# Kernel tuning notes

Measured on AMD Instinct MI355X. Metric: run time of the kernel, lower is better.

## Reference

```python
import jax, jax.numpy as jnp
import numpy as np
import math

N_HEADS = 16
D_HEAD = 64
D_MODEL = 1024
ROPE_THETA = 10000.0


def setup_inputs() -> dict:
    key = jax.random.key(0)
    k1, k2, k3 = jax.random.split(key, 3)
    B, T = 2, 2048
    x = jax.random.normal(k1, (B, T, D_MODEL), dtype=jnp.float32)
    # torch Linear(in, out) weight has shape (out, in); store transposed (in, out)
    # so forward is x @ w. Scale like default init to keep activations sane.
    w_qkv = jax.random.normal(k2, (D_MODEL, 3 * D_MODEL), dtype=jnp.float32) / math.sqrt(D_MODEL)
    w_o = jax.random.normal(k3, (D_MODEL, D_MODEL), dtype=jnp.float32) / math.sqrt(D_MODEL)
    return {"x": x, "w_qkv": w_qkv, "w_o": w_o}


def _build_rope(T, dtype):
    inv_freq = 1.0 / (ROPE_THETA ** (jnp.arange(0, D_HEAD, 2, dtype=jnp.float32) / D_HEAD))
    t = jnp.arange(T, dtype=jnp.float32)
    freqs = jnp.outer(t, inv_freq)            # [T, D_HEAD/2]
    emb = jnp.concatenate([freqs, freqs], -1)  # [T, D_HEAD]
    return jnp.cos(emb).astype(dtype), jnp.sin(emb).astype(dtype)


def _apply_rope(x, cos, sin):
    # x: [B, T, H, D_HEAD]; cos/sin broadcast as [1, T, 1, D_HEAD]
    x1, x2 = jnp.split(x, 2, axis=-1)
    rotated = jnp.concatenate([-x2, x1], axis=-1)
    return x * cos + rotated * sin


def reference(x, w_qkv, w_o):
    B, T, D = x.shape
    qkv = (x @ w_qkv).reshape(B, T, 3, N_HEADS, D_HEAD)
    q, k, v = qkv[:, :, 0], qkv[:, :, 1], qkv[:, :, 2]  # [B, T, H, Dh]
    cos, sin = _build_rope(T, x.dtype)
    cos = cos[None, :, None, :]
    sin = sin[None, :, None, :]
    q = _apply_rope(q, cos, sin)
    k = _apply_rope(k, cos, sin)
    scale = 1.0 / math.sqrt(D_HEAD)
    # full [B, H, T, T] scores (faithful to the manual matmul-softmax-matmul)
    attn = jnp.einsum("bthd,bshd->bhts", q, k) * scale
    attn = jax.nn.softmax(attn, axis=-1)
    out = jnp.einsum("bhts,bshd->bthd", attn, v).reshape(B, T, D)
    return out @ w_o
```

## Files before the change

### kernel.cpp

```cpp
#include <hip/hip_runtime.h>
#include <cstdint>

typedef unsigned short ushort_t;
typedef __attribute__((ext_vector_type(8))) short v8s;
typedef __attribute__((ext_vector_type(4))) short v4s;
typedef __attribute__((ext_vector_type(2))) unsigned v2u;
typedef __attribute__((ext_vector_type(4))) float v4f;

#define MFMA(a, b, c) __builtin_amdgcn_mfma_f32_16x16x32_bf16(a, b, c, 0, 0, 0)
#define QSCALE 0.18033688011112042f

__device__ __forceinline__ float bf2f(ushort_t u) {
    union { unsigned u; float f; } x; x.u = ((unsigned)u) << 16; return x.f;
}
__device__ __forceinline__ short f2bf(float f) {
    union { float f; unsigned u; } x; x.f = f;
    unsigned r = x.u + 0x7fffu + ((x.u >> 16) & 1u);
    return (short)(r >> 16);
}

__global__ void detect_dtype(const unsigned* __restrict__ x, int* __restrict__ flag) {
    __shared__ int cnt;
    if (threadIdx.x == 0) cnt = 0;
    __syncthreads();
    unsigned w = x[threadIdx.x];
    int e = (w >> 7) & 0xFF;
    int hit = ((e >= 96 && e <= 135) || (w & 0xFFFFu) == 0) ? 1 : 0;
    atomicAdd(&cnt, hit);
    __syncthreads();
    if (threadIdx.x == 0) *flag = (cnt >= 160) ? 1 : 0;
}

__global__ __launch_bounds__(256) void cvt_x(const void* __restrict__ xin,
                                             ushort_t* __restrict__ xb,
                                             const int* __restrict__ flagp, int n8) {
    int i = blockIdx.x * 256 + threadIdx.x;
    if (i >= n8) return;
    if (*flagp) {
        ((v8s*)xb)[i] = ((const v8s*)xin)[i];
    } else {
        const float* xf = (const float*)xin + (size_t)i * 8;
        v8s o;
        #pragma unroll
        for (int j = 0; j < 8; ++j) o[j] = f2bf(xf[j]);
        ((v8s*)xb)[i] = o;
    }
}

__global__ __launch_bounds__(256) void cvt_transpose(const void* __restrict__ in,
                                                     ushort_t* __restrict__ out,
                                                     const int* __restrict__ flagp,
                                                     int R, int C) {
    __shared__ ushort_t tile[32][33];
    int bx = blockIdx.x * 32, by = blockIdx.y * 32;
    int tx = threadIdx.x, ty = threadIdx.y;
    int isbf = *flagp;
    for (int i = ty; i < 32; i += 8) {
        size_t idx = (size_t)(by + i) * C + bx + tx;
        tile[i][tx] = isbf ? ((const ushort_t*)in)[idx]
                           : (ushort_t)f2bf(((const float*)in)[idx]);
    }
    __syncthreads();
    for (int i = ty; i < 32; i += 8) out[(size_t)(bx + i) * R + by + tx] = tile[tx][i];
}

__global__ __launch_bounds__(256) void rope_table(float* __restrict__ tab) {
    int idx = blockIdx.x * 256 + threadIdx.x;
    int t = idx >> 5, d = idx & 31;
    float inv_freq = __expf(-(float)d * 0.28782313662425575f);
    float ang = (float)t * inv_freq;
    float sn, cs;
    sincosf(ang, &sn, &cs);
    tab[t * 64 + d]      = bf2f((ushort_t)f2bf(cs));
    tab[t * 64 + 32 + d] = bf2f((ushort_t)f2bf(sn));
}

template <int MODE>
__global__ __launch_bounds__(256) void gemm_bt(const ushort_t* __restrict__ A,
                                               const ushort_t* __restrict__ BT,
                                               void* __restrict__ C,
                                               const int* __restrict__ flagp,
                                               int M, int N, int K,
                                               ushort_t* __restrict__ Qp,
                                               ushort_t* __restrict__ Kp,
                                               ushort_t* __restrict__ Vp,
                                               const float* __restrict__ tab) {
    __shared__ __align__(16) ushort_t As[128 * 32];
    __shared__ __align__(16) ushort_t Bs[128 * 32];
    int tid = threadIdx.x;
    int lane = tid & 63;
    int lr = lane & 15, lc = lane >> 4;
    int w = tid >> 6;
    int wr = (w >> 1) * 64, wc = (w & 1) * 64;
    int m0 = blockIdx.y * 128, n0 = blockIdx.x * 128;

    int c0 = tid, c1 = tid + 256;
    int r0 = c0 >> 2, s0 = c0 & 3;
    int r1 = c1 >> 2, s1 = c1 & 3;

    v4f acc[4][4] = {};

    for (int kt = 0; kt < K; kt += 32) {
        v8s a0 = *(const v8s*)(A + (size_t)(m0 + r0) * K + kt + s0 * 8);
        v8s a1 = *(const v8s*)(A + (size_t)(m0 + r1) * K + kt + s1 * 8);
        v8s b0 = *(const v8s*)(BT + (size_t)(n0 + r0) * K + kt + s0 * 8);
        v8s b1 = *(const v8s*)(BT + (size_t)(n0 + r1) * K + kt + s1 * 8);
        __syncthreads();
        *(v8s*)(As + (size_t)c0 * 8) = a0;
        *(v8s*)(As + (size_t)c1 * 8) = a1;
        *(v8s*)(Bs + (size_t)c0 * 8) = b0;
        *(v8s*)(Bs + (size_t)c1 * 8) = b1;
        __syncthreads();

        v8s af[4], bfr[4];
        #pragma unroll
        for (int i = 0; i < 4; ++i)
            af[i] = *(const v8s*)(As + (wr + i * 16 + lr) * 32 + lc * 8);
        #pragma unroll
        for (int j = 0; j < 4; ++j)
            bfr[j] = *(const v8s*)(Bs + (wc + j * 16 + lr) * 32 + lc * 8);
        #pragma unroll
        for (int i = 0; i < 4; ++i)
            #pragma unroll
            for (int j = 0; j < 4; ++j)
                acc[i][j] = MFMA(af[i], bfr[j], acc[i][j]);
    }

    if (MODE == 1) {
        int store_f32 = (*flagp == 0);
        #pragma unroll
        for (int i = 0; i < 4; ++i)
            #pragma unroll
            for (int j = 0; j < 4; ++j)
                #pragma unroll
                for (int r = 0; r < 4; ++r) {
                    int row = m0 + wr + i * 16 + lc * 4 + r;
                    int col = n0 + wc + j * 16 + lr;
                    if (store_f32)
                        ((float*)C)[(size_t)row * N + col] = acc[i][j][r];
                    else
                        ((ushort_t*)C)[(size_t)row * N + col] = (ushort_t)f2bf(acc[i][j][r]);
                }
    } else {
        int region = n0 >> 10;
        int h = ((n0 & 1023) + wc) >> 6;
        if (region < 2) {
            const float sc = (region == 0) ? QSCALE : 1.0f;
            ushort_t* dst = (region == 0) ? Qp : Kp;
            #pragma unroll
            for (int i = 0; i < 4; ++i)
                #pragma unroll
                for (int j = 0; j < 2; ++j) {
                    int d = j * 16 + lr;
                    #pragma unroll
                    for (int r = 0; r < 4; ++r) {
                        int tg = m0 + wr + i * 16 + lc * 4 + r;
                        int b = tg >> 11, tt = tg & 2047;
                        float cs = tab[tt * 64 + d], sn = tab[tt * 64 + 32 + d];
                        float x1 = acc[i][j][r], x2 = acc[i][j + 2][r];
                        size_t base = ((size_t)(b * 16 + h) * 2048 + tt) * 64 + d;
                        dst[base]      = (ushort_t)f2bf((x1 * cs - x2 * sn) * sc);
                        dst[base + 32] = (ushort_t)f2bf((x2 * cs + x1 * sn) * sc);
                    }
                }
        } else {
            #pragma unroll
            for (int i = 0; i < 4; ++i)
                #pragma unroll
                for (int j = 0; j < 4; ++j) {
                    int d = j * 16 + lr;
                    int tg0 = m0 + wr + i * 16 + lc * 4;
                    int b = tg0 >> 11, tt = tg0 & 2047;
                    v4s pk;
                    #pragma unroll
                    for (int r = 0; r < 4; ++r) pk[r] = f2bf(acc[i][j][r]);
                    size_t base = (size_t)(b * 16 + h) * 131072 + (size_t)(tt >> 5) * 2048
                                + (size_t)d * 32 + (tt & 31);
                    *(v4s*)(Vp + base) = pk;
                }
        }
    }
}

#define ISSUE_LOAD(dst, ptr) \
    asm volatile("global_load_dwordx4 %0, %1, off" : "=v"(dst) : "v"(ptr))
#define WAIT_VM8(sl) \
    asm volatile("s_waitcnt vmcnt(8)" \
        : "+v"(kf[sl][0][0]), "+v"(kf[sl][0][1]), "+v"(kf[sl][1][0]), "+v"(kf[sl][1][1]), \
          "+v"(vf[sl][0]), "+v"(vf[sl][1]), "+v"(vf[sl][2]), "+v"(vf[sl][3]))
#define WAIT_VM0(sl) \
    asm volatile("s_waitcnt vmcnt(0)" \
        : "+v"(kf[sl][0][0]), "+v"(kf[sl][0][1]), "+v"(kf[sl][1][0]), "+v"(kf[sl][1][1]), \
          "+v"(vf[sl][0]), "+v"(vf[sl][1]), "+v"(vf[sl][2]), "+v"(vf[sl][3]))

__global__ __launch_bounds__(128) void attn(const ushort_t* __restrict__ Qr,
                                            const ushort_t* __restrict__ Kr,
                                            const ushort_t* __restrict__ Vt,
                                            ushort_t* __restrict__ AO) {
    __shared__ __align__(16) ushort_t P[2 * 2560];
    __shared__ __align__(16) float MO[64 * 68];
    __shared__ float Mli[64];
    int tid = threadIdx.x, lane = tid & 63, W = tid >> 6;
    int lr = lane & 15, lc = lane >> 4;
    int L = blockIdx.x;
    int xcd = L & 7, slot = L >> 3;
    int bh = xcd * 4 + (slot >> 5);
    int q0 = (slot & 31) * 64;
    int b = bh >> 4, h = bh & 15;
    const ushort_t* Qb = Qr + ((size_t)bh * 2048 + q0) * 64;
    const ushort_t* Kp = Kr + (size_t)bh * 131072 + (size_t)W * 65536 + lr * 64 + lc * 8;
    const ushort_t* Vp = Vt + (size_t)bh * 131072 + (size_t)W * 65536 + lr * 32 + lc * 8;
    ushort_t* Pw = P + W * 2560;

    v8s qf[4][2];
    #pragma unroll
    for (int jq = 0; jq < 4; ++jq)
        #pragma unroll
        for (int kk = 0; kk < 2; ++kk)
            qf[jq][kk] = *(const v8s*)(Qb + (size_t)(jq * 16 + lr) * 64 + kk * 32 + lc * 8);

    v4f o[4][4] = {};
    float li[4] = {0.f, 0.f, 0.f, 0.f};
    v8s kf[2][2][2], vf[2][4];

    auto issueK = [&](int sl, int stp) {
        #pragma unroll
        for (int hh = 0; hh < 2; ++hh)
            #pragma unroll
            for (int kk = 0; kk < 2; ++kk) {
                const ushort_t* p = Kp + (size_t)stp * 2048 + hh * 1024 + kk * 32;
                if (sl == 0) ISSUE_LOAD(kf[0][hh][kk], p);
                else         ISSUE_LOAD(kf[1][hh][kk], p);
            }
    };
    auto issueV = [&](int sl, int stp) {
        #pragma unroll
        for (int i = 0; i < 4; ++i) {
            const ushort_t* p = Vp + (size_t)stp * 2048 + i * 512;
            if (sl == 0) ISSUE_LOAD(vf[0][i], p);
            else         ISSUE_LOAD(vf[1][i], p);
        }
    };
    auto step = [&](v8s (&kfs)[2][2], v8s (&vfs)[4]) {
        v4f St[2][4] = {};
        #pragma unroll
        for (int hh = 0; hh < 2; ++hh)
            #pragma unroll
            for (int jq = 0; jq < 4; ++jq) {
                St[hh][jq] = MFMA(kfs[hh][0], qf[jq][0], St[hh][jq]);
                St[hh][jq] = MFMA(kfs[hh][1], qf[jq][1], St[hh][jq]);
            }
        #pragma unroll
        for (int jq = 0; jq < 4; ++jq)
            #pragma unroll
            for (int hh = 0; hh < 2; ++hh) {
                #pragma unroll
                for (int r = 0; r < 4; ++r) {
                    float ev = __builtin_amdgcn_exp2f(St[hh][jq][r]);
                    St[hh][jq][r] = ev;
                    li[jq] += ev;
                }
                unsigned d0 = __builtin_amdgcn_perm(__float_as_uint(St[hh][jq][1]),
                                                    __float_as_uint(St[hh][jq][0]), 0x07060302u);
                unsigned d1 = __builtin_amdgcn_perm(__float_as_uint(St[hh][jq][3]),
                                                    __float_as_uint(St[hh][jq][2]), 0x07060302u);
                v2u pk = {d0, d1};
                *(v2u*)(Pw + (jq * 16 + lr) * 40 + hh * 16 + lc * 4) = pk;
            }
        __builtin_amdgcn_s_waitcnt(0xc07f);
        #pragma unroll
        for (int jq = 0; jq < 4; ++jq) {
            v8s pf = *(const v8s*)(Pw + (jq * 16 + lr) * 40 + lc * 8);
            #pragma unroll
            for (int i = 0; i < 4; ++i)
                o[i][jq] = MFMA(vfs[i], pf, o[i][jq]);
        }
    };

    issueK(0, 0); issueV(0, 0);
    issueK(1, 1); issueV(1, 1);
    #pragma unroll 1
    for (int stp = 0; stp < 32; stp += 2) {
        WAIT_VM8(0);
        step(kf[0], vf[0]);
        if (stp + 2 < 32) { issueK(0, stp + 2); issueV(0, stp + 2); }
        if (stp + 3 < 32) { WAIT_VM8(1); } else { WAIT_VM0(1); }
        step(kf[1], vf[1]);
        if (stp + 3 < 32) { issueK(1, stp + 3); issueV(1, stp + 3); }
    }

    #pragma unroll
    for (int jq = 0; jq < 4; ++jq) {
        li[jq] += __shfl_xor(li[jq], 16);
        li[jq] += __shfl_xor(li[jq], 32);
    }
    if (W == 1) {
        #pragma unroll
        for (int jq = 0; jq < 4; ++jq) {
            #pragma unroll
            for (int i = 0; i < 4; ++i)
                *(v4f*)(MO + (jq * 16 + lr) * 68 + i * 16 + lc * 4) = o[i][jq];
            if (lc == 0) Mli[jq * 16 + lr] = li[jq];
        }
    }
    __syncthreads();
    if (W == 0) {
        #pragma unroll
        for (int jq = 0; jq < 4; ++jq) {
            float inv = 1.0f / (li[jq] + Mli[jq * 16 + lr]);
            int t = q0 + jq * 16 + lr;
            #pragma unroll
            for (int i = 0; i < 4; ++i) {
                v4f m = *(const v4f*)(MO + (jq * 16 + lr) * 68 + i * 16 + lc * 4);
                v4s pk;
                #pragma unroll
                for (int r = 0; r < 4; ++r) pk[r] = f2bf((o[i][jq][r] + m[r]) * inv);
                *(v4s*)(AO + (size_t)(b * 2048 + t) * 1024 + h * 64 + i * 16 + lc * 4) = pk;
            }
        }
    }
}

extern "C" void kernel_launch(void* const* d_in, const int* in_sizes, int n_in,
                              void* d_out, int out_size, void* d_ws, size_t ws_size,
                              hipStream_t stream) {
    char* ws = (char*)d_ws;
    int*      flag  = (int*)ws;
    ushort_t* wqkvT = (ushort_t*)(ws + 256);
    ushort_t* woT   = (ushort_t*)(ws + 6291712);
    ushort_t* xb    = (ushort_t*)(ws + 8388864);
    ushort_t* Qr    = (ushort_t*)(ws + 16777472);
    ushort_t* Kr    = (ushort_t*)(ws + 25166080);
    ushort_t* Vt    = (ushort_t*)(ws + 33554688);
    ushort_t* AO    = (ushort_t*)(ws + 41943296);
    float*    tab   = (float*)(ws + 50331904);

    detect_dtype<<<1, 256, 0, stream>>>((const unsigned*)d_in[0], flag);
    rope_table<<<256, 256, 0, stream>>>(tab);
    cvt_x<<<2048, 256, 0, stream>>>(d_in[0], xb, flag, 524288);
    dim3 tb(32, 8);
    cvt_transpose<<<dim3(96, 32), tb, 0, stream>>>(d_in[1], wqkvT, flag, 1024, 3072);
    cvt_transpose<<<dim3(32, 32), tb, 0, stream>>>(d_in[2], woT, flag, 1024, 1024);
    gemm_bt<2><<<dim3(24, 32), 256, 0, stream>>>(xb, wqkvT, nullptr, flag, 4096, 3072, 1024,
                                                 Qr, Kr, Vt, tab);
    attn<<<1024, 128, 0, stream>>>(Qr, Kr, Vt, AO);
    gemm_bt<1><<<dim3(8, 32), 256, 0, stream>>>(AO, woT, d_out, flag, 4096, 1024, 1024,
                                                nullptr, nullptr, nullptr, nullptr);
}
```

Measured before the change: 217.4 us.

## Share K/V tiles across four query waves via double-buffered LDS

Restructures the attention kernel so a 256-thread block processes four 64-query tiles that share K/V tiles staged through swizzled, double-buffered shared memory, with a register prefetch two steps ahead. This replaces per-wave direct global loads that split the key range across two waves, and removes the cross-wave output merge. It aims to cut redundant global/L2 K/V traffic. In exchange it adds an LDS round trip, a block barrier every step, and fewer, larger blocks.

Measured after the change: 218.7 us. No clear change (+0.6%).

```diff
diff --git a/kernel.cpp b/kernel.cpp
--- a/kernel.cpp
+++ b/kernel.cpp
@@ -182,35 +182,30 @@
     }
 }
 
-#define ISSUE_LOAD(dst, ptr) \
-    asm volatile("global_load_dwordx4 %0, %1, off" : "=v"(dst) : "v"(ptr))
-#define WAIT_VM8(sl) \
-    asm volatile("s_waitcnt vmcnt(8)" \
-        : "+v"(kf[sl][0][0]), "+v"(kf[sl][0][1]), "+v"(kf[sl][1][0]), "+v"(kf[sl][1][1]), \
-          "+v"(vf[sl][0]), "+v"(vf[sl][1]), "+v"(vf[sl][2]), "+v"(vf[sl][3]))
-#define WAIT_VM0(sl) \
-    asm volatile("s_waitcnt vmcnt(0)" \
-        : "+v"(kf[sl][0][0]), "+v"(kf[sl][0][1]), "+v"(kf[sl][1][0]), "+v"(kf[sl][1][1]), \
-          "+v"(vf[sl][0]), "+v"(vf[sl][1]), "+v"(vf[sl][2]), "+v"(vf[sl][3]))
-
-__global__ __launch_bounds__(128) void attn(const ushort_t* __restrict__ Qr,
+__global__ __launch_bounds__(256) void attn(const ushort_t* __restrict__ Qr,
                                             const ushort_t* __restrict__ Kr,
                                             const ushort_t* __restrict__ Vt,
                                             ushort_t* __restrict__ AO) {
-    __shared__ __align__(16) ushort_t P[2 * 2560];
-    __shared__ __align__(16) float MO[64 * 68];
-    __shared__ float Mli[64];
+    __shared__ __align__(16) ushort_t Ks[2][2048];
+    __shared__ __align__(16) ushort_t Vs[2][2048];
+    __shared__ __align__(16) ushort_t P[4][2560];
     int tid = threadIdx.x, lane = tid & 63, W = tid >> 6;
     int lr = lane & 15, lc = lane >> 4;
     int L = blockIdx.x;
-    int xcd = L & 7, slot = L >> 3;
-    int bh = xcd * 4 + (slot >> 5);
-    int q0 = (slot & 31) * 64;
+    int bh = (L & 7) * 4 + ((L >> 3) & 3);
+    int qt = L >> 5;
+    int q0 = qt * 256 + W * 64;
     int b = bh >> 4, h = bh & 15;
     const ushort_t* Qb = Qr + ((size_t)bh * 2048 + q0) * 64;
-    const ushort_t* Kp = Kr + (size_t)bh * 131072 + (size_t)W * 65536 + lr * 64 + lc * 8;
-    const ushort_t* Vp = Vt + (size_t)bh * 131072 + (size_t)W * 65536 + lr * 32 + lc * 8;
-    ushort_t* Pw = P + W * 2560;
+    const ushort_t* Kb = Kr + (size_t)bh * 131072;
+    const ushort_t* Vb = Vt + (size_t)bh * 131072;
+    ushort_t* Pw = P[W];
+
+    int krow = tid >> 3, kchk = tid & 7;
+    const ushort_t* Kg = Kb + (size_t)krow * 64 + kchk * 8;
+    int klds = krow * 64 + (kchk ^ (krow & 7)) * 8;
+    const ushort_t* Vg = Vb + (size_t)tid * 8;
+    int vlds = tid * 8;
 
     v8s qf[4][2];
     #pragma unroll
@@ -221,35 +216,49 @@
 
     v4f o[4][4] = {};
     float li[4] = {0.f, 0.f, 0.f, 0.f};
-    v8s kf[2][2][2], vf[2][4];
-
-    auto issueK = [&](int sl, int stp) {
+
+    v8s kreg = *(const v8s*)(Kg);
+    v8s vreg = *(const v8s*)(Vg);
+    *(v8s*)(&Ks[0][klds]) = kreg;
+    *(v8s*)(&Vs[0][vlds]) = vreg;
+    kreg = *(const v8s*)(Kg + 2048);
+    vreg = *(const v8s*)(Vg + 2048);
+    __syncthreads();
+
+    #pragma unroll 1
+    for (int t = 0; t < 64; ++t) {
+        int p = t & 1;
+        const ushort_t* Kl = Ks[p];
+        const ushort_t* Vl = Vs[p];
+
+        v8s kf[2][2], vf[4];
         #pragma unroll
         for (int hh = 0; hh < 2; ++hh)
             #pragma unroll
-            for (int kk = 0; kk < 2; ++kk) {
-                const ushort_t* p = Kp + (size_t)stp * 2048 + hh * 1024 + kk * 32;
-                if (sl == 0) ISSUE_LOAD(kf[0][hh][kk], p);
-                else         ISSUE_LOAD(kf[1][hh][kk], p);
+            for (int kk = 0; kk < 2; ++kk)
+                kf[hh][kk] = *(const v8s*)(Kl + (hh * 16 + lr) * 64 + (((kk * 4 + lc) ^ (lr & 7)) * 8));
+        #pragma unroll
+        for (int i = 0; i < 4; ++i)
+            vf[i] = *(const v8s*)(Vl + (i * 16 + lr) * 32 + lc * 8);
+
+        v4f St[2][4] = {};
+        #pragma unroll
+        for (int hh = 0; hh < 2; ++hh)
+            #pragma unroll
+            for (int jq = 0; jq < 4; ++jq) {
+                St[hh][jq] = MFMA(kf[hh][0], qf[jq][0], St[hh][jq]);
+                St[hh][jq] = MFMA(kf[hh][1], qf[jq][1], St[hh][jq]);
             }
-    };
-    auto issueV = [&](int sl, int stp) {
-        #pragma unroll
-        for (int i = 0; i < 4; ++i) {
-            const ushort_t* p = Vp + (size_t)stp * 2048 + i * 512;
-            if (sl == 0) ISSUE_LOAD(vf[0][i], p);
-            else         ISSUE_LOAD(vf[1][i], p);
-        }
-    };
-    auto step = [&](v8s (&kfs)[2][2], v8s (&vfs)[4]) {
-        v4f St[2][4] = {};
-        #pragma unroll
-        for (int hh = 0; hh < 2; ++hh)
-            #pragma unroll
-            for (int jq = 0; jq < 4; ++jq) {
-                St[hh][jq] = MFMA(kfs[hh][0], qf[jq][0], St[hh][jq]);
-                St[hh][jq] = MFMA(kfs[hh][1], qf[jq][1], St[hh][jq]);
-            }
+
+        if (t + 1 < 64) {
+            *(v8s*)(&Ks[p ^ 1][klds]) = kreg;
+            *(v8s*)(&Vs[p ^ 1][vlds]) = vreg;
+        }
+        if (t + 2 < 64) {
+            kreg = *(const v8s*)(Kg + (size_t)(t + 2) * 2048);
+            vreg = *(const v8s*)(Vg + (size_t)(t + 2) * 2048);
+        }
+
         #pragma unroll
         for (int jq = 0; jq < 4; ++jq)
             #pragma unroll
@@ -273,50 +282,23 @@
             v8s pf = *(const v8s*)(Pw + (jq * 16 + lr) * 40 + lc * 8);
             #pragma unroll
             for (int i = 0; i < 4; ++i)
-                o[i][jq] = MFMA(vfs[i], pf, o[i][jq]);
-        }
-    };
-
-    issueK(0, 0); issueV(0, 0);
-    issueK(1, 1); issueV(1, 1);
-    #pragma unroll 1
-    for (int stp = 0; stp < 32; stp += 2) {
-        WAIT_VM8(0);
-        step(kf[0], vf[0]);
-        if (stp + 2 < 32) { issueK(0, stp + 2); issueV(0, stp + 2); }
-        if (stp + 3 < 32) { WAIT_VM8(1); } else { WAIT_VM0(1); }
-        step(kf[1], vf[1]);
-        if (stp + 3 < 32) { issueK(1, stp + 3); issueV(1, stp + 3); }
+                o[i][jq] = MFMA(vf[i], pf, o[i][jq]);
+        }
+        __syncthreads();
     }
 
     #pragma unroll
     for (int jq = 0; jq < 4; ++jq) {
         li[jq] += __shfl_xor(li[jq], 16);
         li[jq] += __shfl_xor(li[jq], 32);
-    }
-    if (W == 1) {
-        #pragma unroll
-        for (int jq = 0; jq < 4; ++jq) {
-            #pragma unroll
-            for (int i = 0; i < 4; ++i)
-                *(v4f*)(MO + (jq * 16 + lr) * 68 + i * 16 + lc * 4) = o[i][jq];
-            if (lc == 0) Mli[jq * 16 + lr] = li[jq];
-        }
-    }
-    __syncthreads();
-    if (W == 0) {
-        #pragma unroll
-        for (int jq = 0; jq < 4; ++jq) {
-            float inv = 1.0f / (li[jq] + Mli[jq * 16 + lr]);
-            int t = q0 + jq * 16 + lr;
-            #pragma unroll
-            for (int i = 0; i < 4; ++i) {
-                v4f m = *(const v4f*)(MO + (jq * 16 + lr) * 68 + i * 16 + lc * 4);
-                v4s pk;
-                #pragma unroll
-                for (int r = 0; r < 4; ++r) pk[r] = f2bf((o[i][jq][r] + m[r]) * inv);
-                *(v4s*)(AO + (size_t)(b * 2048 + t) * 1024 + h * 64 + i * 16 + lc * 4) = pk;
-            }
+        float inv = 1.0f / li[jq];
+        int t = q0 + jq * 16 + lr;
+        #pragma unroll
+        for (int i = 0; i < 4; ++i) {
+            v4s pk;
+            #pragma unroll
+            for (int r = 0; r < 4; ++r) pk[r] = f2bf(o[i][jq][r] * inv);
+            *(v4s*)(AO + (size_t)(b * 2048 + t) * 1024 + h * 64 + i * 16 + lc * 4) = pk;
         }
     }
 }
@@ -343,7 +325,7 @@
     cvt_transpose<<<dim3(32, 32), tb, 0, stream>>>(d_in[2], woT, flag, 1024, 1024);
     gemm_bt<2><<<dim3(24, 32), 256, 0, stream>>>(xb, wqkvT, nullptr, flag, 4096, 3072, 1024,
                                                  Qr, Kr, Vt, tab);
-    attn<<<1024, 128, 0, stream>>>(Qr, Kr, Vt, AO);
+    attn<<<256, 256, 0, stream>>>(Qr, Kr, Vt, AO);
     gemm_bt<1><<<dim3(8, 32), 256, 0, stream>>>(AO, woT, d_out, flag, 4096, 1024, 1024,
                                                 nullptr, nullptr, nullptr, nullptr);
 }
```
